# Kernel tuning notes

Hardware: AMD Instinct MI355X
Metric: run time of the kernel (lower is better)

Reference implementation:

```python
import math
import jax, jax.numpy as jnp
import numpy as np

B, L, C_S, C_Z, H, C, PQK, PV = 1, 768, 256, 128, 8, 32, 4, 8
OUT_DIM = H * C + H * PV * 3 + H * PV + H * 4  # 544
EPS_LN = 1e-5


def _ln(x, w, b):
    m = jnp.mean(x, axis=-1, keepdims=True)
    v = jnp.mean((x - m) ** 2, axis=-1, keepdims=True)
    return (x - m) * jax.lax.rsqrt(v + EPS_LN) * w + b


def setup_inputs() -> dict:
    key = jax.random.key(0)
    ks = jax.random.split(key, 16)
    f = lambda k, shape, s=1.0: jax.random.normal(k, shape, jnp.float32) * s
    w = 0.05  # weight init scale
    return {
        "s": f(ks[0], (B, L, C_S)),
        "z": f(ks[1], (B, L, L, C_Z)),
        "R": f(ks[2], (B, L, 3, 3)),
        "t": f(ks[3], (B, L, 3)),
        "mask": jnp.ones((B, L), jnp.float32),
        "ln_s_w": jnp.ones((C_S,), jnp.float32),
        "ln_s_b": jnp.zeros((C_S,), jnp.float32),
        "ln_z_w": jnp.ones((C_Z,), jnp.float32),
        "ln_z_b": jnp.zeros((C_Z,), jnp.float32),
        "Wq": f(ks[4], (C_S, H * C), w),
        "Wk": f(ks[5], (C_S, H * C), w),
        "Wv": f(ks[6], (C_S, H * C), w),
        "W_pair_bias": f(ks[7], (C_Z, H), w),
        "Wq_pts": f(ks[8], (C_S, H * PQK * 3), w),
        "Wk_pts": f(ks[9], (C_S, H * PQK * 3), w),
        "Wv_pts": f(ks[10], (C_S, H * PV * 3), w),
        "point_weights": f(ks[11], (H,), 0.1),
        "W_pair_out": f(ks[12], (C_Z, H * 4), w),
        "W_out": f(ks[13], (OUT_DIM, C_S), w),
        "b_out": jnp.zeros((C_S,), jnp.float32),
    }


def reference(s, z, R, t, mask, ln_s_w, ln_s_b, ln_z_w, ln_z_b,
              Wq, Wk, Wv, W_pair_bias, Wq_pts, Wk_pts, Wv_pts,
              point_weights, W_pair_out, W_out, b_out):
    s = _ln(s, ln_s_w, ln_s_b)               # [B,L,c_s]
    z = _ln(z, ln_z_w, ln_z_b)               # [B,L,L,c_z]

    q = (s @ Wq).reshape(B, L, H, C)
    k = (s @ Wk).reshape(B, L, H, C)
    v = (s @ Wv).reshape(B, L, H, C)

    scalar_logits = jnp.einsum('bihc,bjhc->bhij', q, k) / math.sqrt(C)
    pair_bias = jnp.transpose(z @ W_pair_bias, (0, 3, 1, 2))  # [B,H,L,L]

    q_pts = (s @ Wq_pts).reshape(B, L, H, PQK, 3)
    k_pts = (s @ Wk_pts).reshape(B, L, H, PQK, 3)
    v_pts = (s @ Wv_pts).reshape(B, L, H, PV, 3)

    t_b = t[:, :, None, None, :]
    apply_T = lambda p: jnp.einsum('blxy,blhpy->blhpx', R, p) + t_b
    q_pts_g = apply_T(q_pts)  # [B,L,H,Pqk,3]
    k_pts_g = apply_T(k_pts)
    v_pts_g = apply_T(v_pts)  # [B,L,H,Pv,3]

    diff = q_pts_g[:, :, None] - k_pts_g[:, None]          # [B,L,L,H,P,3]
    sq_dist = jnp.sum(diff ** 2, axis=(-1, -2))            # [B,L,L,H]
    sq_dist = jnp.transpose(sq_dist, (0, 3, 1, 2))         # [B,H,L,L]

    pw = jax.nn.softplus(point_weights)[None, :, None, None]
    logits = scalar_logits + pair_bias - 0.5 * pw * sq_dist

    pair_mask = mask[:, :, None] * mask[:, None, :]
    logits = jnp.where(pair_mask[:, None] == 0, -1e9, logits)
    attn = jax.nn.softmax(logits, axis=-1)                 # [B,H,L,L]

    scalar_out = jnp.einsum('bhij,bjhc->bihc', attn, v).reshape(B, L, H * C)

    pair_v = (z @ W_pair_out).reshape(B, L, L, H, 4)
    pair_out = jnp.einsum('bhij,bijhd->bihd', attn, pair_v).reshape(B, L, H * 4)

    pt_out_g = jnp.einsum('bhij,bjhpc->bihpc', attn, v_pts_g)    # [B,L,H,Pv,3]
    # invert transform: R^T (x - t)
    pt_out_l = jnp.einsum('blxy,blhpx->blhpy', R, pt_out_g - t_b)
    point_out = pt_out_l.reshape(B, L, H * PV * 3)
    point_norms = jnp.sqrt(jnp.sum(pt_out_l ** 2, axis=-1) + 1e-8).reshape(B, L, H * PV)

    s_update = jnp.concatenate([scalar_out, point_out, point_norms, pair_out], axis=-1)
    s_update = s_update @ W_out + b_out
    s_update = s_update * mask[:, :, None]
    return s_update, attn
```

## Files before the change

kernel.cpp:

```cpp
#include <hip/hip_runtime.h>
#include <math.h>

#define L 768
#define CS 256
#define CZ 128
#define H 8
#define LL (L*L)

typedef __attribute__((ext_vector_type(8))) short bf16x8;
typedef __attribute__((ext_vector_type(4))) float floatx4;

static __device__ __forceinline__ unsigned short f2bf(float f){
  unsigned int u = __float_as_uint(f);
  unsigned int r = (u + 0x7fffu + ((u >> 16) & 1u)) >> 16;
  return (unsigned short)r;
}

__global__ void k_ln_s(const float* __restrict__ s, const float* __restrict__ w,
                       const float* __restrict__ b, float* __restrict__ out) {
  int i = blockIdx.x, t = threadIdx.x;
  __shared__ float red[256];
  float x = s[i*CS + t];
  red[t] = x; __syncthreads();
  for (int s2=128; s2>0; s2>>=1){ if (t<s2) red[t]+=red[t+s2]; __syncthreads(); }
  float mean = red[0] * (1.0f/CS); __syncthreads();
  float d = x - mean;
  red[t] = d*d; __syncthreads();
  for (int s2=128; s2>0; s2>>=1){ if (t<s2) red[t]+=red[t+s2]; __syncthreads(); }
  float var = red[0] * (1.0f/CS);
  float rstd = rsqrtf(var + 1e-5f);
  out[i*CS+t] = d*rstd*w[t] + b[t];
}

__global__ void k_proj(const float* __restrict__ s_n,
                       const float* __restrict__ Wq, const float* __restrict__ Wk, const float* __restrict__ Wv,
                       const float* __restrict__ Wqp, const float* __restrict__ Wkp, const float* __restrict__ Wvp,
                       const float* __restrict__ R, const float* __restrict__ t,
                       float* __restrict__ q, float* __restrict__ kT, float* __restrict__ v,
                       float* __restrict__ qpg, float* __restrict__ kpgT, float* __restrict__ vpg) {
  int i = blockIdx.x, tid = threadIdx.x;
  __shared__ float srow[256];
  __shared__ float qraw[96], kraw[96], vraw[192];
  __shared__ float Rl[9], tl[3];
  srow[tid] = s_n[i*CS + tid];
  if (tid < 9) Rl[tid] = R[i*9 + tid];
  if (tid >= 16 && tid < 19) tl[tid-16] = t[i*3 + (tid-16)];
  __syncthreads();
  float aq=0.f, ak=0.f, av=0.f;
  #pragma unroll 4
  for (int c=0;c<256;c++){ float sv=srow[c];
    aq = fmaf(sv, Wq[c*256+tid], aq);
    ak = fmaf(sv, Wk[c*256+tid], ak);
    av = fmaf(sv, Wv[c*256+tid], av); }
  q[i*256+tid]=aq; kT[(size_t)tid*L + i]=ak; v[i*256+tid]=av;
  if (tid < 96){
    float a1=0.f, a2=0.f;
    #pragma unroll 4
    for (int c=0;c<256;c++){ float sv=srow[c];
      a1 = fmaf(sv, Wqp[c*96+tid], a1);
      a2 = fmaf(sv, Wkp[c*96+tid], a2); }
    qraw[tid]=a1; kraw[tid]=a2;
  }
  if (tid < 192){
    float a3=0.f;
    #pragma unroll 4
    for (int c=0;c<256;c++) a3 = fmaf(srow[c], Wvp[c*192+tid], a3);
    vraw[tid]=a3;
  }
  __syncthreads();
  if (tid < 32){
    int b0 = tid*3;
    float px=qraw[b0], py=qraw[b0+1], pz=qraw[b0+2];
    #pragma unroll
    for (int x=0;x<3;x++)
      qpg[i*96 + b0 + x] = Rl[x*3]*px + Rl[x*3+1]*py + Rl[x*3+2]*pz + tl[x];
  } else if (tid < 64){
    int b0 = (tid-32)*3;
    float px=kraw[b0], py=kraw[b0+1], pz=kraw[b0+2];
    #pragma unroll
    for (int x=0;x<3;x++)
      kpgT[(size_t)(b0+x)*L + i] = Rl[x*3]*px + Rl[x*3+1]*py + Rl[x*3+2]*pz + tl[x];
  } else if (tid < 128){
    int b0 = (tid-64)*3;
    float px=vraw[b0], py=vraw[b0+1], pz=vraw[b0+2];
    #pragma unroll
    for (int x=0;x<3;x++)
      vpg[i*192 + b0 + x] = Rl[x*3]*px + Rl[x*3+1]*py + Rl[x*3+2]*pz + tl[x];
  }
}

__global__ void k_prep(const float* __restrict__ lzw, const float* __restrict__ lzb,
                       const float* __restrict__ Wpb, const float* __restrict__ Wpo,
                       unsigned short* __restrict__ Bpack, float* __restrict__ uv) {
  int tid = threadIdx.x;
  if (tid < 48){
    int o = tid;
    float uo = 0.f, vo = 0.f;
    for (int c=0;c<128;c++){
      float W = (o<8) ? Wpb[c*8+o] : ((o<40) ? Wpo[c*32+o-8] : 0.f);
      uo = fmaf(lzw[c], W, uo);
      vo = fmaf(lzb[c], W, vo);
    }
    uv[o] = uo; uv[48+o] = vo;
  }
  for (int idx=tid; idx<6144; idx+=256){
    int jj = idx & 7, lane = (idx>>3)&63, kb = (idx>>9)&3, nt = idx>>11;
    int c = kb*32 + (lane>>4)*8 + jj;
    int o = nt*16 + (lane&15);
    float W = (o<8) ? Wpb[c*8+o] : ((o<40) ? Wpo[c*32+o-8] : 0.f);
    Bpack[idx] = f2bf(lzw[c]*W);
  }
}

__global__ __launch_bounds__(256) void k_zfuse(
    const float* __restrict__ z, const unsigned short* __restrict__ Bpack,
    const float* __restrict__ uv, float* __restrict__ pb, float* __restrict__ pv) {
  int i = blockIdx.x, jt = blockIdx.y, tid = threadIdx.x;
  int j0 = jt * 64;
  __shared__ unsigned short znb[64*136];
  __shared__ float smean[64], srstd[64];
  __shared__ float su[48], sv[48];

  if (tid < 48){ su[tid] = uv[tid]; sv[tid] = uv[48+tid]; }

  const float4* zb4 = (const float4*)(z + ((size_t)i*L + j0)*CZ);
  int lane31 = tid & 31;
  #pragma unroll
  for (int k=0;k<8;k++){
    int idx4 = k*256 + tid;
    float4 v4 = zb4[idx4];
    int r = idx4 >> 5, c4 = idx4 & 31;
    float sm = v4.x+v4.y+v4.z+v4.w;
    float sq = v4.x*v4.x+v4.y*v4.y+v4.z*v4.z+v4.w*v4.w;
    #pragma unroll
    for (int d=1; d<32; d<<=1){ sm += __shfl_xor(sm,d); sq += __shfl_xor(sq,d); }
    if (lane31 == 0){
      float mean = sm*(1.f/128.f);
      float var  = sq*(1.f/128.f) - mean*mean;
      smean[r] = mean; srstd[r] = rsqrtf(var + 1e-5f);
    }
    ushort4 pk = make_ushort4(f2bf(v4.x), f2bf(v4.y), f2bf(v4.z), f2bf(v4.w));
    *(ushort4*)&znb[r*136 + c4*4] = pk;
  }
  __syncthreads();

  int w = tid >> 6;
  int lane = tid & 63;
  int n16 = lane & 15, quad = lane >> 4;

  floatx4 acc0 = {0,0,0,0}, acc1 = {0,0,0,0}, acc2 = {0,0,0,0};
  const bf16x8* Bp = (const bf16x8*)Bpack;
  #pragma unroll
  for (int kb=0; kb<4; kb++){
    bf16x8 afrag = *(const bf16x8*)&znb[(w*16 + n16)*136 + kb*32 + quad*8];
    bf16x8 b0 = Bp[(0*4+kb)*64 + lane];
    bf16x8 b1 = Bp[(1*4+kb)*64 + lane];
    bf16x8 b2 = Bp[(2*4+kb)*64 + lane];
    acc0 = __builtin_amdgcn_mfma_f32_16x16x32_bf16(afrag, b0, acc0, 0,0,0);
    acc1 = __builtin_amdgcn_mfma_f32_16x16x32_bf16(afrag, b1, acc1, 0,0,0);
    acc2 = __builtin_amdgcn_mfma_f32_16x16x32_bf16(afrag, b2, acc2, 0,0,0);
  }

  #pragma unroll
  for (int nt=0; nt<3; nt++){
    int o = nt*16 + n16;
    if (o >= 40) continue;
    float uo = su[o], vo = sv[o];
    const floatx4 acc = (nt==0) ? acc0 : (nt==1) ? acc1 : acc2;
    #pragma unroll
    for (int reg=0; reg<4; reg++){
      int jl = w*16 + quad*4 + reg;
      int j = j0 + jl;
      float val = srstd[jl]*(acc[reg] - smean[jl]*uo) + vo;
      if (o < 8) pb[(size_t)o*LL + (size_t)i*L + j] = val;
      else       pv[((size_t)i*L + j)*32 + (o-8)] = val;
    }
  }
}

__global__ __launch_bounds__(256) void k_attn_fused(
    const float* __restrict__ q, const float* __restrict__ kT, const float* __restrict__ v,
    const float* __restrict__ qpg, const float* __restrict__ kpgT, const float* __restrict__ vpg,
    float* __restrict__ pb_attn, const float* __restrict__ pv,
    const float* __restrict__ R, const float* __restrict__ t,
    const float* __restrict__ point_weights, const float* __restrict__ mask,
    float* __restrict__ su_pre) {
  int i = blockIdx.x, tid = threadIdx.x;
  int h = tid >> 5, jl = tid & 31;

  __shared__ float sml[8*776];
  __shared__ float sm_q[256];
  __shared__ float sm_qp[96];
  __shared__ float sm_mask[768];
  __shared__ float sm_ptg[192];
  __shared__ float sm_ptl[192];
  __shared__ float Rl[9], tl[3];

  sm_q[tid] = q[i*256 + tid];
  if (tid < 96) sm_qp[tid] = qpg[i*96 + tid];
  if (tid >= 96 && tid < 105) Rl[tid-96] = R[i*9 + (tid-96)];
  if (tid >= 112 && tid < 115) tl[tid-112] = t[i*3 + (tid-112)];
  #pragma unroll
  for (int rr=0; rr<3; rr++) sm_mask[rr*256 + tid] = mask[rr*256 + tid];
  __syncthreads();

  float pw = log1pf(__expf(point_weights[h]));
  float mi = mask[i];
  float qreg[32];
  #pragma unroll
  for (int c=0;c<32;c++) qreg[c] = sm_q[h*32+c];
  float qp_reg[12];
  #pragma unroll
  for (int pc=0;pc<12;pc++) qp_reg[pc] = sm_qp[h*12+pc];

  const float* kTb  = kT  + (size_t)(h*32)*L + jl;
  const float* kpTb = kpgT + (size_t)(h*12)*L + jl;
  const float* pbb  = pb_attn + (size_t)h*LL + (size_t)i*L + jl;

  float lg[24];
  for (int jt=0; jt<24; jt++){
    int joff = jt*32;
    float dot = 0.f;
    #pragma unroll
    for (int c=0;c<32;c++) dot = fmaf(qreg[c], kTb[(size_t)c*L + joff], dot);
    float sq = 0.f;
    #pragma unroll
    for (int pc=0;pc<12;pc++){ float d = qp_reg[pc] - kpTb[(size_t)pc*L + joff]; sq = fmaf(d,d,sq); }
    float lgv = dot*0.17677669529663687f + pbb[joff] - 0.5f*pw*sq;
    if (mi*sm_mask[joff+jl] == 0.f) lgv = -1e9f;
    lg[jt] = lgv;
  }

  float m = -1e30f;
  #pragma unroll
  for (int jt=0; jt<24; jt++) m = fmaxf(m, lg[jt]);
  #pragma unroll
  for (int d=1; d<32; d<<=1) m = fmaxf(m, __shfl_xor(m, d));
  float ssum = 0.f;
  #pragma unroll
  for (int jt=0; jt<24; jt++){ float e = __expf(lg[jt]-m); lg[jt]=e; ssum+=e; }
  #pragma unroll
  for (int d=1; d<32; d<<=1) ssum += __shfl_xor(ssum, d);
  float inv = 1.0f/ssum;
  float* pbw = pb_attn + (size_t)h*LL + (size_t)i*L + jl;
  #pragma unroll
  for (int jt=0; jt<24; jt++){
    float a = lg[jt]*inv;
    sml[h*776 + jt*32 + jl] = a;
    pbw[jt*32] = a;
  }
  __syncthreads();

  int h2 = (tid < 192) ? (tid/24) : ((tid < 224) ? ((tid-192)>>2) : 0);
  const float* src2; int stride2;
  if (tid < 192)      { src2 = vpg + tid;                                stride2 = 192; }
  else if (tid < 224) { src2 = pv + (size_t)i*L*32 + (tid-192);          stride2 = 32;  }
  else                { src2 = vpg + 0;                                  stride2 = 0;   }
  const float* vb = v + tid;
  const float* smlA = sml + h*776;
  const float* smlB = sml + h2*776;
  float acc_s = 0.f, acc2 = 0.f;
  #pragma unroll 4
  for (int j=0; j<768; j++){
    float a  = smlA[j];
    acc_s = fmaf(a, vb[(size_t)j*256], acc_s);
    float a2 = smlB[j];
    acc2 = fmaf(a2, src2[(size_t)j*stride2], acc2);
  }
  su_pre[i*544 + tid] = acc_s;
  if (tid < 192) sm_ptg[tid] = acc2;
  else if (tid < 224) su_pre[i*544 + 512 + (tid-192)] = acc2;
  __syncthreads();

  if (tid < 192){
    int hh = tid/24, rem = tid%24, p = rem/3, y = rem%3;
    float lv = 0.f;
    #pragma unroll
    for (int x=0;x<3;x++) lv = fmaf(Rl[x*3+y], sm_ptg[hh*24+p*3+x]-tl[x], lv);
    sm_ptl[tid] = lv;
    su_pre[i*544 + 256 + tid] = lv;
  }
  __syncthreads();
  if (tid < 64){
    float a0=sm_ptl[tid*3], a1=sm_ptl[tid*3+1], a2=sm_ptl[tid*3+2];
    su_pre[i*544 + 448 + tid] = sqrtf(a0*a0+a1*a1+a2*a2 + 1e-8f);
  }
}

__global__ void k_out(const float* __restrict__ su_pre, const float* __restrict__ W_out,
                      const float* __restrict__ b_out, const float* __restrict__ mask,
                      float* __restrict__ out) {
  int i = blockIdx.x, tid = threadIdx.x;
  __shared__ float srow[544];
  for (int idx=tid; idx<544; idx+=256) srow[idx] = su_pre[i*544+idx];
  __syncthreads();
  float acc = b_out[tid];
  #pragma unroll 4
  for (int c=0;c<544;c++) acc = fmaf(srow[c], W_out[c*256+tid], acc);
  out[i*256+tid] = acc * mask[i];
}

extern "C" void kernel_launch(void* const* d_in, const int* in_sizes, int n_in,
                              void* d_out, int out_size, void* d_ws, size_t ws_size,
                              hipStream_t stream) {
  const float* s    = (const float*)d_in[0];
  const float* z    = (const float*)d_in[1];
  const float* R    = (const float*)d_in[2];
  const float* t    = (const float*)d_in[3];
  const float* mask = (const float*)d_in[4];
  const float* lsw  = (const float*)d_in[5];
  const float* lsb  = (const float*)d_in[6];
  const float* lzw  = (const float*)d_in[7];
  const float* lzb  = (const float*)d_in[8];
  const float* Wq   = (const float*)d_in[9];
  const float* Wk   = (const float*)d_in[10];
  const float* Wv   = (const float*)d_in[11];
  const float* Wpb  = (const float*)d_in[12];
  const float* Wqp  = (const float*)d_in[13];
  const float* Wkp  = (const float*)d_in[14];
  const float* Wvp  = (const float*)d_in[15];
  const float* pwts = (const float*)d_in[16];
  const float* Wpo  = (const float*)d_in[17];
  const float* Wout = (const float*)d_in[18];
  const float* bout = (const float*)d_in[19];

  float* out0 = (float*)d_out;
  float* attn = out0 + (size_t)L*CS;

  float* ws   = (float*)d_ws;
  float* s_n  = ws;                        size_t off = (size_t)L*CS;
  float* q    = ws + off;                  off += (size_t)L*CS;
  float* kT   = ws + off;                  off += (size_t)L*CS;
  float* v    = ws + off;                  off += (size_t)L*CS;
  float* qpg  = ws + off;                  off += (size_t)L*96;
  float* kpgT = ws + off;                  off += (size_t)L*96;
  float* vpg  = ws + off;                  off += (size_t)L*192;
  float* pv   = ws + off;                  off += (size_t)LL*32;
  float* su   = ws + off;                  off += (size_t)L*544;
  unsigned short* Bpack = (unsigned short*)(ws + off); off += 3072;
  float* uv   = ws + off;                  off += 96;

  k_prep<<<1, 256, 0, stream>>>(lzw, lzb, Wpb, Wpo, Bpack, uv);
  k_ln_s<<<L, 256, 0, stream>>>(s, lsw, lsb, s_n);
  k_proj<<<L, 256, 0, stream>>>(s_n, Wq, Wk, Wv, Wqp, Wkp, Wvp, R, t,
                                q, kT, v, qpg, kpgT, vpg);
  k_zfuse<<<dim3(L, L/64), 256, 0, stream>>>(z, Bpack, uv, attn, pv);
  k_attn_fused<<<L, 256, 0, stream>>>(q, kT, v, qpg, kpgT, vpg, attn, pv,
                                      R, t, pwts, mask, su);
  k_out<<<L, 256, 0, stream>>>(su, Wout, bout, mask, out0);
}
```

Measured before the change: 785.2 us.

## Widen projection, z-fusion and attention-value tiles for more register reuse

```diff
diff --git a/kernel.cpp b/kernel.cpp
--- a/kernel.cpp
+++ b/kernel.cpp
@@ -38,54 +38,70 @@
                        const float* __restrict__ R, const float* __restrict__ t,
                        float* __restrict__ q, float* __restrict__ kT, float* __restrict__ v,
                        float* __restrict__ qpg, float* __restrict__ kpgT, float* __restrict__ vpg) {
-  int i = blockIdx.x, tid = threadIdx.x;
-  __shared__ float srow[256];
-  __shared__ float qraw[96], kraw[96], vraw[192];
-  __shared__ float Rl[9], tl[3];
-  srow[tid] = s_n[i*CS + tid];
-  if (tid < 9) Rl[tid] = R[i*9 + tid];
-  if (tid >= 16 && tid < 19) tl[tid-16] = t[i*3 + (tid-16)];
-  __syncthreads();
-  float aq=0.f, ak=0.f, av=0.f;
+  int i0 = blockIdx.x*2, tid = threadIdx.x;
+  __shared__ float srow[2][256];
+  __shared__ float qraw[2][96], kraw[2][96], vraw[2][192];
+  __shared__ float Rl[2][9], tl[2][3];
+  srow[0][tid] = s_n[i0*CS + tid];
+  srow[1][tid] = s_n[(i0+1)*CS + tid];
+  if (tid < 18) Rl[tid/9][tid%9] = R[i0*9 + tid];
+  if (tid >= 24 && tid < 30) tl[(tid-24)/3][(tid-24)%3] = t[i0*3 + (tid-24)];
+  __syncthreads();
+  float aq0=0.f, ak0=0.f, av0=0.f, aq1=0.f, ak1=0.f, av1=0.f;
   #pragma unroll 4
-  for (int c=0;c<256;c++){ float sv=srow[c];
-    aq = fmaf(sv, Wq[c*256+tid], aq);
-    ak = fmaf(sv, Wk[c*256+tid], ak);
-    av = fmaf(sv, Wv[c*256+tid], av); }
-  q[i*256+tid]=aq; kT[(size_t)tid*L + i]=ak; v[i*256+tid]=av;
+  for (int c=0;c<256;c++){
+    float s0=srow[0][c], s1=srow[1][c];
+    float wq=Wq[c*256+tid], wk=Wk[c*256+tid], wv=Wv[c*256+tid];
+    aq0=fmaf(s0,wq,aq0); aq1=fmaf(s1,wq,aq1);
+    ak0=fmaf(s0,wk,ak0); ak1=fmaf(s1,wk,ak1);
+    av0=fmaf(s0,wv,av0); av1=fmaf(s1,wv,av1);
+  }
+  q[i0*256+tid]=aq0; q[(i0+1)*256+tid]=aq1;
+  kT[(size_t)tid*L + i0]=ak0; kT[(size_t)tid*L + i0+1]=ak1;
+  v[i0*256+tid]=av0; v[(i0+1)*256+tid]=av1;
   if (tid < 96){
-    float a1=0.f, a2=0.f;
+    float a10=0.f,a20=0.f,a11=0.f,a21=0.f;
     #pragma unroll 4
-    for (int c=0;c<256;c++){ float sv=srow[c];
-      a1 = fmaf(sv, Wqp[c*96+tid], a1);
-      a2 = fmaf(sv, Wkp[c*96+tid], a2); }
-    qraw[tid]=a1; kraw[tid]=a2;
+    for (int c=0;c<256;c++){
+      float s0=srow[0][c], s1=srow[1][c];
+      float w1=Wqp[c*96+tid], w2=Wkp[c*96+tid];
+      a10=fmaf(s0,w1,a10); a11=fmaf(s1,w1,a11);
+      a20=fmaf(s0,w2,a20); a21=fmaf(s1,w2,a21);
+    }
+    qraw[0][tid]=a10; qraw[1][tid]=a11; kraw[0][tid]=a20; kraw[1][tid]=a21;
   }
   if (tid < 192){
-    float a3=0.f;
+    float a30=0.f,a31=0.f;
     #pragma unroll 4
-    for (int c=0;c<256;c++) a3 = fmaf(srow[c], Wvp[c*192+tid], a3);
-    vraw[tid]=a3;
-  }
-  __syncthreads();
-  if (tid < 32){
-    int b0 = tid*3;
-    float px=qraw[b0], py=qraw[b0+1], pz=qraw[b0+2];
-    #pragma unroll
-    for (int x=0;x<3;x++)
-      qpg[i*96 + b0 + x] = Rl[x*3]*px + Rl[x*3+1]*py + Rl[x*3+2]*pz + tl[x];
-  } else if (tid < 64){
-    int b0 = (tid-32)*3;
-    float px=kraw[b0], py=kraw[b0+1], pz=kraw[b0+2];
-    #pragma unroll
-    for (int x=0;x<3;x++)
-      kpgT[(size_t)(b0+x)*L + i] = Rl[x*3]*px + Rl[x*3+1]*py + Rl[x*3+2]*pz + tl[x];
-  } else if (tid < 128){
-    int b0 = (tid-64)*3;
-    float px=vraw[b0], py=vraw[b0+1], pz=vraw[b0+2];
-    #pragma unroll
-    for (int x=0;x<3;x++)
-      vpg[i*192 + b0 + x] = Rl[x*3]*px + Rl[x*3+1]*py + Rl[x*3+2]*pz + tl[x];
+    for (int c=0;c<256;c++){
+      float w3=Wvp[c*192+tid];
+      a30=fmaf(srow[0][c],w3,a30); a31=fmaf(srow[1][c],w3,a31);
+    }
+    vraw[0][tid]=a30; vraw[1][tid]=a31;
+  }
+  __syncthreads();
+  #pragma unroll
+  for (int rr=0; rr<2; rr++){
+    int i = i0 + rr;
+    if (tid < 32){
+      int b0 = tid*3;
+      float px=qraw[rr][b0], py=qraw[rr][b0+1], pz=qraw[rr][b0+2];
+      #pragma unroll
+      for (int x=0;x<3;x++)
+        qpg[i*96 + b0 + x] = Rl[rr][x*3]*px + Rl[rr][x*3+1]*py + Rl[rr][x*3+2]*pz + tl[rr][x];
+    } else if (tid < 64){
+      int b0 = (tid-32)*3;
+      float px=kraw[rr][b0], py=kraw[rr][b0+1], pz=kraw[rr][b0+2];
+      #pragma unroll
+      for (int x=0;x<3;x++)
+        kpgT[(size_t)(b0+x)*L + i] = Rl[rr][x*3]*px + Rl[rr][x*3+1]*py + Rl[rr][x*3+2]*pz + tl[rr][x];
+    } else if (tid < 128){
+      int b0 = (tid-64)*3;
+      float px=vraw[rr][b0], py=vraw[rr][b0+1], pz=vraw[rr][b0+2];
+      #pragma unroll
+      for (int x=0;x<3;x++)
+        vpg[i*192 + b0 + x] = Rl[rr][x*3]*px + Rl[rr][x*3+1]*py + Rl[rr][x*3+2]*pz + tl[rr][x];
+    }
   }
 }
 
@@ -116,64 +132,64 @@
     const float* __restrict__ z, const unsigned short* __restrict__ Bpack,
     const float* __restrict__ uv, float* __restrict__ pb, float* __restrict__ pv) {
   int i = blockIdx.x, jt = blockIdx.y, tid = threadIdx.x;
-  int j0 = jt * 64;
-  __shared__ unsigned short znb[64*136];
-  __shared__ float smean[64], srstd[64];
-  __shared__ float su[48], sv[48];
-
-  if (tid < 48){ su[tid] = uv[tid]; sv[tid] = uv[48+tid]; }
-
-  const float4* zb4 = (const float4*)(z + ((size_t)i*L + j0)*CZ);
-  int lane31 = tid & 31;
-  #pragma unroll
-  for (int k=0;k<8;k++){
-    int idx4 = k*256 + tid;
-    float4 v4 = zb4[idx4];
-    int r = idx4 >> 5, c4 = idx4 & 31;
-    float sm = v4.x+v4.y+v4.z+v4.w;
-    float sq = v4.x*v4.x+v4.y*v4.y+v4.z*v4.z+v4.w*v4.w;
-    #pragma unroll
-    for (int d=1; d<32; d<<=1){ sm += __shfl_xor(sm,d); sq += __shfl_xor(sq,d); }
-    if (lane31 == 0){
-      float mean = sm*(1.f/128.f);
-      float var  = sq*(1.f/128.f) - mean*mean;
-      smean[r] = mean; srstd[r] = rsqrtf(var + 1e-5f);
-    }
+  int j0 = jt * 128;
+  __shared__ unsigned short znb[128*136];
+  __shared__ float smean[128], srstd[128];
+
+  int lane = tid & 63;
+  const bf16x8* Bp = (const bf16x8*)Bpack;
+  bf16x8 bfr[3][4];
+  #pragma unroll
+  for (int nt=0; nt<3; nt++)
+    #pragma unroll
+    for (int kb=0; kb<4; kb++)
+      bfr[nt][kb] = Bp[(nt*4+kb)*64 + lane];
+
+  int row = tid >> 1, sub = tid & 1;
+  const float4* zrow = (const float4*)(z + ((size_t)i*L + j0 + row)*CZ);
+  float sm = 0.f, sq = 0.f;
+  #pragma unroll 8
+  for (int kk=0; kk<16; kk++){
+    float4 v4 = zrow[sub + 2*kk];
+    sm += (v4.x+v4.y)+(v4.z+v4.w);
+    sq = fmaf(v4.x,v4.x, fmaf(v4.y,v4.y, fmaf(v4.z,v4.z, fmaf(v4.w,v4.w, sq))));
     ushort4 pk = make_ushort4(f2bf(v4.x), f2bf(v4.y), f2bf(v4.z), f2bf(v4.w));
-    *(ushort4*)&znb[r*136 + c4*4] = pk;
-  }
-  __syncthreads();
+    *(ushort4*)&znb[row*136 + (sub+2*kk)*4] = pk;
+  }
+  sm += __shfl_xor(sm,1); sq += __shfl_xor(sq,1);
+  if (sub == 0){
+    float mean = sm*(1.f/128.f);
+    float var  = sq*(1.f/128.f) - mean*mean;
+    smean[row] = mean; srstd[row] = rsqrtf(var + 1e-5f);
+  }
 
   int w = tid >> 6;
-  int lane = tid & 63;
   int n16 = lane & 15, quad = lane >> 4;
-
-  floatx4 acc0 = {0,0,0,0}, acc1 = {0,0,0,0}, acc2 = {0,0,0,0};
-  const bf16x8* Bp = (const bf16x8*)Bpack;
-  #pragma unroll
-  for (int kb=0; kb<4; kb++){
-    bf16x8 afrag = *(const bf16x8*)&znb[(w*16 + n16)*136 + kb*32 + quad*8];
-    bf16x8 b0 = Bp[(0*4+kb)*64 + lane];
-    bf16x8 b1 = Bp[(1*4+kb)*64 + lane];
-    bf16x8 b2 = Bp[(2*4+kb)*64 + lane];
-    acc0 = __builtin_amdgcn_mfma_f32_16x16x32_bf16(afrag, b0, acc0, 0,0,0);
-    acc1 = __builtin_amdgcn_mfma_f32_16x16x32_bf16(afrag, b1, acc1, 0,0,0);
-    acc2 = __builtin_amdgcn_mfma_f32_16x16x32_bf16(afrag, b2, acc2, 0,0,0);
-  }
-
-  #pragma unroll
-  for (int nt=0; nt<3; nt++){
-    int o = nt*16 + n16;
-    if (o >= 40) continue;
-    float uo = su[o], vo = sv[o];
-    const floatx4 acc = (nt==0) ? acc0 : (nt==1) ? acc1 : acc2;
-    #pragma unroll
-    for (int reg=0; reg<4; reg++){
-      int jl = w*16 + quad*4 + reg;
-      int j = j0 + jl;
-      float val = srstd[jl]*(acc[reg] - smean[jl]*uo) + vo;
-      if (o < 8) pb[(size_t)o*LL + (size_t)i*L + j] = val;
-      else       pv[((size_t)i*L + j)*32 + (o-8)] = val;
+  #pragma unroll
+  for (int mt2=0; mt2<2; mt2++){
+    int mt = w*2 + mt2;
+    floatx4 acc0 = {0,0,0,0}, acc1 = {0,0,0,0}, acc2 = {0,0,0,0};
+    #pragma unroll
+    for (int kb=0; kb<4; kb++){
+      bf16x8 afrag = *(const bf16x8*)&znb[(mt*16 + n16)*136 + kb*32 + quad*8];
+      acc0 = __builtin_amdgcn_mfma_f32_16x16x32_bf16(afrag, bfr[0][kb], acc0, 0,0,0);
+      acc1 = __builtin_amdgcn_mfma_f32_16x16x32_bf16(afrag, bfr[1][kb], acc1, 0,0,0);
+      acc2 = __builtin_amdgcn_mfma_f32_16x16x32_bf16(afrag, bfr[2][kb], acc2, 0,0,0);
+    }
+    #pragma unroll
+    for (int nt=0; nt<3; nt++){
+      int o = nt*16 + n16;
+      if (o >= 40) continue;
+      float uo = uv[o], vo = uv[48+o];
+      const floatx4 acc = (nt==0) ? acc0 : (nt==1) ? acc1 : acc2;
+      #pragma unroll
+      for (int reg=0; reg<4; reg++){
+        int jl = mt*16 + quad*4 + reg;
+        int j = j0 + jl;
+        float val = srstd[jl]*(acc[reg] - smean[jl]*uo) + vo;
+        if (o < 8) pb[(size_t)o*LL + (size_t)i*L + j] = val;
+        else       pv[((size_t)i*L + j)*32 + (o-8)] = val;
+      }
     }
   }
 }
@@ -251,25 +267,22 @@
   }
   __syncthreads();
 
-  int h2 = (tid < 192) ? (tid/24) : ((tid < 224) ? ((tid-192)>>2) : 0);
-  const float* src2; int stride2;
-  if (tid < 192)      { src2 = vpg + tid;                                stride2 = 192; }
-  else if (tid < 224) { src2 = pv + (size_t)i*L*32 + (tid-192);          stride2 = 32;  }
-  else                { src2 = vpg + 0;                                  stride2 = 0;   }
-  const float* vb = v + tid;
-  const float* smlA = sml + h*776;
-  const float* smlB = sml + h2*776;
-  float acc_s = 0.f, acc2 = 0.f;
-  #pragma unroll 4
+  const float2* src; int str; const float* smlB;
+  if (tid < 128)      { src = (const float2*)v + tid;                         str = 128; smlB = sml + (tid>>4)*776; }
+  else if (tid < 224) { int e2=(tid-128)*2; src = (const float2*)vpg + (tid-128); str = 96; smlB = sml + (e2/24)*776; }
+  else if (tid < 240) { int e2=(tid-224)*2; src = (const float2*)(pv + (size_t)i*L*32) + (tid-224); str = 16; smlB = sml + (e2>>2)*776; }
+  else                { src = (const float2*)v; str = 0; smlB = sml; }
+  float2 acc = {0.f, 0.f};
+  #pragma unroll 8
   for (int j=0; j<768; j++){
-    float a  = smlA[j];
-    acc_s = fmaf(a, vb[(size_t)j*256], acc_s);
-    float a2 = smlB[j];
-    acc2 = fmaf(a2, src2[(size_t)j*stride2], acc2);
-  }
-  su_pre[i*544 + tid] = acc_s;
-  if (tid < 192) sm_ptg[tid] = acc2;
-  else if (tid < 224) su_pre[i*544 + 512 + (tid-192)] = acc2;
+    float a = smlB[j];
+    float2 vv = src[(size_t)j*str];
+    acc.x = fmaf(a, vv.x, acc.x);
+    acc.y = fmaf(a, vv.y, acc.y);
+  }
+  if (tid < 128)      *(float2*)&su_pre[i*544 + tid*2] = acc;
+  else if (tid < 224) { int e2=(tid-128)*2; sm_ptg[e2] = acc.x; sm_ptg[e2+1] = acc.y; }
+  else if (tid < 240) *(float2*)&su_pre[i*544 + 512 + (tid-224)*2] = acc;
   __syncthreads();
 
   if (tid < 192){
@@ -342,9 +355,9 @@
 
   k_prep<<<1, 256, 0, stream>>>(lzw, lzb, Wpb, Wpo, Bpack, uv);
   k_ln_s<<<L, 256, 0, stream>>>(s, lsw, lsb, s_n);
-  k_proj<<<L, 256, 0, stream>>>(s_n, Wq, Wk, Wv, Wqp, Wkp, Wvp, R, t,
-                                q, kT, v, qpg, kpgT, vpg);
-  k_zfuse<<<dim3(L, L/64), 256, 0, stream>>>(z, Bpack, uv, attn, pv);
+  k_proj<<<L/2, 256, 0, stream>>>(s_n, Wq, Wk, Wv, Wqp, Wkp, Wvp, R, t,
+                                  q, kT, v, qpg, kpgT, vpg);
+  k_zfuse<<<dim3(L, L/128), 256, 0, stream>>>(z, Bpack, uv, attn, pv);
   k_attn_fused<<<L, 256, 0, stream>>>(q, kT, v, qpg, kpgT, vpg, attn, pv,
                                       R, t, pwts, mask, su);
   k_out<<<L, 256, 0, stream>>>(su, Wout, bout, mask, out0);
```

Result: no change. 776.7 us (-1.1%).
